# Kernel optimization log

Hardware: AMD Instinct MI355X
Metric: run time of the kernel (lower is better)

The kernel has to match this reference:

```python
import jax, jax.numpy as jnp
import numpy as np

B, IN, H, OUT = 256, 512, 1024, 512
S, Wd, SH = 512, 256, 3          # memory_slots, memory_width, shift_range
P_READ = Wd + 2 + SH + 1         # key, beta, gate, shift(3), gamma
P_WRITE = P_READ + 2 * Wd        # + erase, add


def setup_inputs() -> dict:
    key = jax.random.key(0)
    ks = jax.random.split(key, 8)
    sc = 0.02
    return {
        "x": jax.random.normal(ks[0], (B, IN), jnp.float32),
        "W_ih": jax.random.normal(ks[1], (4 * H, IN + Wd), jnp.float32) * sc,
        "b_ih": jnp.zeros((4 * H,), jnp.float32),
        "W_hh": jax.random.normal(ks[2], (4 * H, H), jnp.float32) * sc,
        "b_hh": jnp.zeros((4 * H,), jnp.float32),
        "W_read": jax.random.normal(ks[3], (P_READ, H), jnp.float32) * sc,
        "b_read": jnp.zeros((P_READ,), jnp.float32),
        "W_write": jax.random.normal(ks[4], (P_WRITE, H), jnp.float32) * sc,
        "b_write": jnp.zeros((P_WRITE,), jnp.float32),
        "W_out": jax.random.normal(ks[5], (OUT, H + Wd), jnp.float32) * sc,
        "b_out": jnp.zeros((OUT,), jnp.float32),
        "mem_bias": jax.random.normal(ks[6], (S, Wd), jnp.float32) * sc,
    }


def _content_address(key_v, beta, memory):
    # cosine similarity of key [B,Wd] vs memory [B,S,Wd], eps=1e-8 like torch
    num = jnp.einsum('bw,bsw->bs', key_v, memory)
    kn = jnp.maximum(jnp.linalg.norm(key_v, axis=1, keepdims=True), 1e-8)
    mn = jnp.maximum(jnp.linalg.norm(memory, axis=2), 1e-8)
    sim = num / (kn * mn) * beta[:, None]
    return jax.nn.softmax(sim, axis=1)


def _address(p, prev_w, memory):
    # content_and_location addressing for a single head
    key_v = p[:, :Wd]
    beta = jax.nn.softplus(p[:, Wd])
    gate = jax.nn.sigmoid(p[:, Wd + 1])
    shift = jax.nn.softmax(p[:, Wd + 2:Wd + 2 + SH], axis=1)
    gamma = 1.0 + jax.nn.softplus(p[:, Wd + 2 + SH])
    cw = _content_address(key_v, beta, memory)
    g = gate[:, None]
    gw = g * cw + (1.0 - g) * prev_w  # interpolation gate
    # circular shift: shifted[pos] = s0*w[pos-1] + s1*w[pos] + s2*w[pos+1]
    sw = (shift[:, 0:1] * jnp.roll(gw, 1, axis=1)
          + shift[:, 1:2] * gw
          + shift[:, 2:3] * jnp.roll(gw, -1, axis=1))
    sp = sw ** gamma[:, None]  # sharpening
    return sp / (jnp.sum(sp, axis=1, keepdims=True) + 1e-6)


def reference(x, W_ih, b_ih, W_hh, b_hh, W_read, b_read, W_write, b_write, W_out, b_out, mem_bias):
    Bb = x.shape[0]
    # init_state (prev_state=None path)
    memory = jnp.broadcast_to(mem_bias[None], (Bb, S, Wd))
    w0 = jnp.zeros((Bb, S), x.dtype).at[:, 0].set(1.0)
    rv = jnp.zeros((Bb, Wd), x.dtype)
    h = jnp.zeros((Bb, H), x.dtype)
    c = jnp.zeros((Bb, H), x.dtype)
    # LSTMCell controller
    inp = jnp.concatenate([x, rv], axis=1)
    gates = inp @ W_ih.T + b_ih + h @ W_hh.T + b_hh
    i, f, g, o = jnp.split(gates, 4, axis=1)
    c = jax.nn.sigmoid(f) * c + jax.nn.sigmoid(i) * jnp.tanh(g)
    h = jax.nn.sigmoid(o) * jnp.tanh(c)
    # read head addressing (1 head)
    rp = h @ W_read.T + b_read
    read_w = _address(rp, w0, memory)
    # write head addressing + erase/add (1 head)
    wp = h @ W_write.T + b_write
    write_w = _address(wp, w0, memory)
    erase = jax.nn.sigmoid(wp[:, P_READ:P_READ + Wd])
    add = jnp.tanh(wp[:, P_READ + Wd:])
    memory = memory * (1.0 - write_w[:, :, None] * erase[:, None, :]) + write_w[:, :, None] * add[:, None, :]
    # read after write
    rv = jnp.einsum('bsw,bs->bw', memory, read_w)
    out = jnp.concatenate([h, rv], axis=1) @ W_out.T + b_out
    return out
```

## Files before the change

### kernel.cpp

```cpp
#include <hip/hip_runtime.h>
#include <hip/hip_bf16.h>
#include <math.h>

#define BB   256
#define INW  512
#define HH   1024
#define OUTW 512
#define SS   512
#define WD   256
#define P_READ  262
#define P_WRITE 774
#define RW_LD   1056
#define W_OFF   272

typedef __attribute__((ext_vector_type(8))) short bf16x8;
typedef __attribute__((ext_vector_type(4))) float f32x4;

__device__ __forceinline__ float sigmoidf(float x) { return 1.f / (1.f + expf(-x)); }
__device__ __forceinline__ float softplusf(float x) { return (x > 20.f) ? x : log1pf(expf(x)); }

#define N_WIH (3072*512)
#define N_WRW (RW_LD*1024)
#define N_WO  (512*1280)
#define N_X   (256*512)
#define N_MB  (512*256)
#define N_MT  (256*512)
#define N_BIA 3072
#define N_BRW RW_LD
#define N_TOT (N_WIH+N_WRW+N_WO+N_X+N_MB+N_MT+N_BIA+N_BRW)
#define NB_ELEM ((N_TOT + 255) / 256)

__global__ __launch_bounds__(256)
void convert_all(const float* __restrict__ W_ih, const float* __restrict__ b_ih,
                 const float* __restrict__ b_hh,
                 const float* __restrict__ W_read, const float* __restrict__ b_read,
                 const float* __restrict__ W_write, const float* __restrict__ b_write,
                 const float* __restrict__ W_out, const float* __restrict__ x,
                 const float* __restrict__ mem,
                 __hip_bfloat16* __restrict__ Wih_c, __hip_bfloat16* __restrict__ Wrw_p,
                 __hip_bfloat16* __restrict__ Wo_b, __hip_bfloat16* __restrict__ x_b,
                 __hip_bfloat16* __restrict__ mem_b, __hip_bfloat16* __restrict__ memT_b,
                 float* __restrict__ bias_c, float* __restrict__ bias_rw,
                 float* __restrict__ mem_norm)
{
    if (blockIdx.x >= NB_ELEM) {
        __shared__ float red[4];
        int s = blockIdx.x - NB_ELEM;
        float v = mem[(size_t)s * WD + threadIdx.x];
        float vv = v * v;
        #pragma unroll
        for (int off = 32; off > 0; off >>= 1) vv += __shfl_down(vv, off, 64);
        int wid = threadIdx.x >> 6;
        if ((threadIdx.x & 63) == 0) red[wid] = vv;
        __syncthreads();
        if (threadIdx.x == 0)
            mem_norm[s] = fmaxf(sqrtf(red[0] + red[1] + red[2] + red[3]), 1e-8f);
        return;
    }
    long i = (long)blockIdx.x * 256 + threadIdx.x;
    if (i >= N_TOT) return;
    if (i < N_WIH) {
        int r = (int)(i >> 9), c = (int)(i & 511);
        int sr = r < 1024 ? r : r + 1024;
        Wih_c[i] = __float2bfloat16(W_ih[(size_t)sr * 768 + c]);
        return;
    }
    i -= N_WIH;
    if (i < N_WRW) {
        int r = (int)(i >> 10), c = (int)(i & 1023);
        float v = 0.f;
        if (r < W_OFF) { if (r < P_READ) v = W_read[(size_t)r * 1024 + c]; }
        else { int wr = r - W_OFF; if (wr < P_WRITE) v = W_write[(size_t)wr * 1024 + c]; }
        Wrw_p[i] = __float2bfloat16(v);
        return;
    }
    i -= N_WRW;
    if (i < N_WO) { Wo_b[i] = __float2bfloat16(W_out[i]); return; }
    i -= N_WO;
    if (i < N_X)  { x_b[i] = __float2bfloat16(x[i]); return; }
    i -= N_X;
    if (i < N_MB) { mem_b[i] = __float2bfloat16(mem[i]); return; }
    i -= N_MB;
    if (i < N_MT) {
        int w = (int)(i >> 9), s = (int)(i & 511);
        memT_b[i] = __float2bfloat16(mem[(size_t)s * 256 + w]);
        return;
    }
    i -= N_MT;
    if (i < N_BIA) {
        int r = (int)i;
        int sr = r < 1024 ? r : r + 1024;
        bias_c[r] = b_ih[sr] + b_hh[sr];
        return;
    }
    i -= N_BIA;
    {
        int r = (int)i;
        float v = 0.f;
        if (r < W_OFF) { if (r < P_READ) v = b_read[r]; }
        else { int wr = r - W_OFF; if (wr < P_WRITE) v = b_write[wr]; }
        bias_rw[r] = v;
    }
}

__global__ __launch_bounds__(64)
void gemm_gates(const __hip_bfloat16* __restrict__ x_b,
                const __hip_bfloat16* __restrict__ Wih_c,
                const float* __restrict__ bias_c,
                __hip_bfloat16* __restrict__ hrv)
{
    const int l = threadIdx.x;
    const int bn = blockIdx.x * 16;
    const int bm = blockIdx.y * 16;
    const int r = l & 15, q = l >> 4;
    const __hip_bfloat16* aptr = x_b + (size_t)(bm + r) * INW + q * 8;
    const __hip_bfloat16* bi = Wih_c + (size_t)(bn + r) * INW + q * 8;
    const __hip_bfloat16* bg = bi + (size_t)1024 * INW;
    const __hip_bfloat16* bo = bi + (size_t)2048 * INW;
    f32x4 ai = {0.f,0.f,0.f,0.f}, ag = ai, ao = ai;
    #pragma unroll
    for (int k = 0; k < INW; k += 32) {
        bf16x8 a = *reinterpret_cast<const bf16x8*>(aptr + k);
        ai = __builtin_amdgcn_mfma_f32_16x16x32_bf16(a, *reinterpret_cast<const bf16x8*>(bi + k), ai, 0, 0, 0);
        ag = __builtin_amdgcn_mfma_f32_16x16x32_bf16(a, *reinterpret_cast<const bf16x8*>(bg + k), ag, 0, 0, 0);
        ao = __builtin_amdgcn_mfma_f32_16x16x32_bf16(a, *reinterpret_cast<const bf16x8*>(bo + k), ao, 0, 0, 0);
    }
    const int j = bn + r;
    const float bii = bias_c[j], big = bias_c[1024 + j], bio = bias_c[2048 + j];
    #pragma unroll
    for (int jj = 0; jj < 4; ++jj) {
        int b = bm + q * 4 + jj;
        float gi = ai[jj] + bii, gg = ag[jj] + big, go = ao[jj] + bio;
        float c = sigmoidf(gi) * tanhf(gg);
        hrv[(size_t)b * 1280 + j] = __float2bfloat16(sigmoidf(go) * tanhf(c));
    }
}

__global__ __launch_bounds__(64)
void gemm_mfma(const __hip_bfloat16* __restrict__ A, int lda,
               const __hip_bfloat16* __restrict__ B, int ldb,
               const float* __restrict__ bias,
               float* __restrict__ C, int ldc, int K,
               __hip_bfloat16* __restrict__ kcopy)
{
    const int l = threadIdx.x;
    const int bn = blockIdx.x * 16;
    const int bm = blockIdx.y * 16;
    const int r = l & 15, q = l >> 4;
    const __hip_bfloat16* aptr = A + (size_t)(bm + r) * lda + q * 8;
    const __hip_bfloat16* bptr = B + (size_t)(bn + r) * ldb + q * 8;
    const int K2 = (K >> 6) << 5;
    f32x4 acc0 = {0.f,0.f,0.f,0.f}, acc1 = acc0;
    #pragma unroll 4
    for (int k = 0; k < K2; k += 32)
        acc0 = __builtin_amdgcn_mfma_f32_16x16x32_bf16(
            *reinterpret_cast<const bf16x8*>(aptr + k),
            *reinterpret_cast<const bf16x8*>(bptr + k), acc0, 0, 0, 0);
    #pragma unroll 4
    for (int k = K2; k < K; k += 32)
        acc1 = __builtin_amdgcn_mfma_f32_16x16x32_bf16(
            *reinterpret_cast<const bf16x8*>(aptr + k),
            *reinterpret_cast<const bf16x8*>(bptr + k), acc1, 0, 0, 0);
    const int col = bn + r;
    const float bv = bias ? bias[col] : 0.f;
    #pragma unroll
    for (int j = 0; j < 4; ++j) {
        int m = bm + q * 4 + j;
        float v = acc0[j] + acc1[j] + bv;
        C[(size_t)m * ldc + col] = v;
        if (kcopy) {
            if (col < WD)
                kcopy[(size_t)m * WD + col] = __float2bfloat16(v);
            else if (col >= W_OFF && col < W_OFF + WD)
                kcopy[(size_t)(256 + m) * WD + (col - W_OFF)] = __float2bfloat16(v);
        }
    }
}

__device__ __forceinline__ void redpair_sum(float& a, float& b, volatile float* redA, volatile float* redB) {
    #pragma unroll
    for (int off = 32; off > 0; off >>= 1) { a += __shfl_down(a, off, 64); b += __shfl_down(b, off, 64); }
    int wid = threadIdx.x >> 6;
    __syncthreads();
    if ((threadIdx.x & 63) == 0) { redA[wid] = a; redB[wid] = b; }
    __syncthreads();
    a = redA[0]+redA[1]+redA[2]+redA[3]+redA[4]+redA[5]+redA[6]+redA[7];
    b = redB[0]+redB[1]+redB[2]+redB[3]+redB[4]+redB[5]+redB[6]+redB[7];
}
__device__ __forceinline__ void redpair_max(float& a, float& b, volatile float* redA, volatile float* redB) {
    #pragma unroll
    for (int off = 32; off > 0; off >>= 1) { a = fmaxf(a, __shfl_down(a, off, 64)); b = fmaxf(b, __shfl_down(b, off, 64)); }
    int wid = threadIdx.x >> 6;
    __syncthreads();
    if ((threadIdx.x & 63) == 0) { redA[wid] = a; redB[wid] = b; }
    __syncthreads();
    a = fmaxf(fmaxf(fmaxf(redA[0],redA[1]),fmaxf(redA[2],redA[3])),fmaxf(fmaxf(redA[4],redA[5]),fmaxf(redA[6],redA[7])));
    b = fmaxf(fmaxf(fmaxf(redB[0],redB[1]),fmaxf(redB[2],redB[3])),fmaxf(fmaxf(redB[4],redB[5]),fmaxf(redB[6],redB[7])));
}

__global__ __launch_bounds__(512)
void address_fused(const float* __restrict__ rpwp, const float* __restrict__ num,
                   const float* __restrict__ mem_norm,
                   __hip_bfloat16* __restrict__ A12, float* __restrict__ t3)
{
    const int b = blockIdx.x;
    const int t = threadIdx.x;
    const float* pr = rpwp + (size_t)b * RW_LD;
    const float* pw = pr + W_OFF;

    __shared__ float redA[8], redB[8];
    __shared__ float bufr[SS], bufw[SS];

    float beta_r  = softplusf(pr[WD]);
    float gate_r  = sigmoidf(pr[WD + 1]);
    float r0 = pr[WD+2], r1 = pr[WD+3], r2 = pr[WD+4];
    float rmx = fmaxf(r0, fmaxf(r1, r2));
    float re0 = expf(r0-rmx), re1 = expf(r1-rmx), re2 = expf(r2-rmx);
    float rinv = 1.f / (re0+re1+re2);
    float shr0 = re0*rinv, shr1 = re1*rinv, shr2 = re2*rinv;
    float gamma_r = 1.f + softplusf(pr[WD + 5]);

    float beta_w  = softplusf(pw[WD]);
    float gate_w  = sigmoidf(pw[WD + 1]);
    float w0 = pw[WD+2], w1 = pw[WD+3], w2 = pw[WD+4];
    float wmx = fmaxf(w0, fmaxf(w1, w2));
    float we0 = expf(w0-wmx), we1 = expf(w1-wmx), we2 = expf(w2-wmx);
    float winv = 1.f / (we0+we1+we2);
    float shw0 = we0*winv, shw1 = we1*winv, shw2 = we2*winv;
    float gamma_w = 1.f + softplusf(pw[WD + 5]);

    {
        float kv = (t < WD) ? pr[t] : pw[t - WD];
        float vv = kv * kv;
        #pragma unroll
        for (int off = 32; off > 0; off >>= 1) vv += __shfl_down(vv, off, 64);
        int wid = t >> 6;
        if ((t & 63) == 0) redA[wid] = vv;
        __syncthreads();
    }
    float knr = fmaxf(sqrtf(redA[0]+redA[1]+redA[2]+redA[3]), 1e-8f);
    float knw = fmaxf(sqrtf(redA[4]+redA[5]+redA[6]+redA[7]), 1e-8f);
    __syncthreads();

    float mni = 1.f / mem_norm[t];
    float sim_r = num[(size_t)b * SS + t]         * mni / knr * beta_r;
    float sim_w = num[(size_t)(256 + b) * SS + t] * mni / knw * beta_w;

    float mr = sim_r, mw = sim_w;
    redpair_max(mr, mw, redA, redB);
    float exr = expf(sim_r - mr), exw = expf(sim_w - mw);
    float sr = exr, sw = exw;
    redpair_sum(sr, sw, redA, redB);
    float cwr = exr / sr, cww = exw / sw;

    float onehot = (t == 0) ? 1.f : 0.f;
    float gwr = gate_r * cwr + (1.f - gate_r) * onehot;
    float gww = gate_w * cww + (1.f - gate_w) * onehot;
    __syncthreads();
    bufr[t] = gwr; bufw[t] = gww;
    __syncthreads();

    int tm = (t + SS - 1) & (SS - 1), tp = (t + 1) & (SS - 1);
    float swr = shr0 * bufr[tm] + shr1 * gwr + shr2 * bufr[tp];
    float sww = shw0 * bufw[tm] + shw1 * gww + shw2 * bufw[tp];

    float spr = powf(swr, gamma_r), spw = powf(sww, gamma_w);
    float ssr = spr, ssw = spw;
    redpair_sum(ssr, ssw, redA, redB);
    float rfin = spr / (ssr + 1e-6f);
    float wfin = spw / (ssw + 1e-6f);

    float prod = rfin * wfin;
    A12[(size_t)b * SS + t] = __float2bfloat16(rfin);
    A12[(size_t)(256 + b) * SS + t] = __float2bfloat16(prod);
    float tp3 = prod, dummy = 0.f;
    redpair_sum(tp3, dummy, redA, redB);
    if (t == 0) t3[b] = tp3;
}

__global__ __launch_bounds__(64)
void gemm_t12rv(const __hip_bfloat16* __restrict__ A12,
                const __hip_bfloat16* __restrict__ memT_b,
                const float* __restrict__ rpwp, const float* __restrict__ t3,
                __hip_bfloat16* __restrict__ hrv)
{
    const int l = threadIdx.x;
    const int bn = blockIdx.x * 16;
    const int bm = blockIdx.y * 16;
    const int r = l & 15, q = l >> 4;
    const __hip_bfloat16* a1 = A12 + (size_t)(bm + r) * SS + q * 8;
    const __hip_bfloat16* a2 = a1 + (size_t)256 * SS;
    const __hip_bfloat16* bp = memT_b + (size_t)(bn + r) * SS + q * 8;
    f32x4 acc1 = {0.f,0.f,0.f,0.f}, acc2 = acc1;
    #pragma unroll
    for (int k = 0; k < SS; k += 32) {
        bf16x8 bb = *reinterpret_cast<const bf16x8*>(bp + k);
        acc1 = __builtin_amdgcn_mfma_f32_16x16x32_bf16(*reinterpret_cast<const bf16x8*>(a1 + k), bb, acc1, 0, 0, 0);
        acc2 = __builtin_amdgcn_mfma_f32_16x16x32_bf16(*reinterpret_cast<const bf16x8*>(a2 + k), bb, acc2, 0, 0, 0);
    }
    const int w = bn + r;
    #pragma unroll
    for (int j = 0; j < 4; ++j) {
        int b = bm + q * 4 + j;
        const float* row = rpwp + (size_t)b * RW_LD;
        float e = sigmoidf(row[W_OFF + P_READ + w]);
        float a = tanhf(row[W_OFF + P_READ + WD + w]);
        float rv = acc1[j] - e * acc2[j] + a * t3[b];
        hrv[(size_t)b * 1280 + 1024 + w] = __float2bfloat16(rv);
    }
}

extern "C" void kernel_launch(void* const* d_in, const int* in_sizes, int n_in,
                              void* d_out, int out_size, void* d_ws, size_t ws_size,
                              hipStream_t stream)
{
    const float* x       = (const float*)d_in[0];
    const float* W_ih    = (const float*)d_in[1];
    const float* b_ih    = (const float*)d_in[2];
    const float* b_hh    = (const float*)d_in[4];
    const float* W_read  = (const float*)d_in[5];
    const float* b_read  = (const float*)d_in[6];
    const float* W_write = (const float*)d_in[7];
    const float* b_write = (const float*)d_in[8];
    const float* W_out   = (const float*)d_in[9];
    const float* b_out   = (const float*)d_in[10];
    const float* mem     = (const float*)d_in[11];

    float* ws = (float*)d_ws;
    float* rpwp     = ws;
    float* num      = ws + 270336;
    float* bias_c   = ws + 532480;
    float* bias_rw  = ws + 535552;
    float* mem_norm = ws + 536608;
    float* t3       = ws + 537120;
    __hip_bfloat16* bfb = (__hip_bfloat16*)(ws + 537376);
    __hip_bfloat16* x_b    = bfb;
    __hip_bfloat16* Wih_c  = bfb + 131072;
    __hip_bfloat16* Wrw_p  = bfb + 1703936;
    __hip_bfloat16* Wo_b   = bfb + 2785280;
    __hip_bfloat16* mem_b  = bfb + 3440640;
    __hip_bfloat16* memT_b = bfb + 3571712;
    __hip_bfloat16* A12    = bfb + 3702784;
    __hip_bfloat16* hrv    = bfb + 3964928;
    __hip_bfloat16* keys   = bfb + 4292608;
    float* out = (float*)d_out;

    convert_all<<<NB_ELEM + SS, 256, 0, stream>>>(
        W_ih, b_ih, b_hh, W_read, b_read, W_write, b_write, W_out, x, mem,
        Wih_c, Wrw_p, Wo_b, x_b, mem_b, memT_b, bias_c, bias_rw, mem_norm);
    gemm_gates<<<dim3(64, 16), 64, 0, stream>>>(x_b, Wih_c, bias_c, hrv);
    gemm_mfma<<<dim3(66, 16), 64, 0, stream>>>(hrv, 1280, Wrw_p, HH, bias_rw,
                                               rpwp, RW_LD, HH, keys);
    gemm_mfma<<<dim3(32, 32), 64, 0, stream>>>(keys, WD, mem_b, WD, nullptr,
                                               num, SS, WD, nullptr);
    address_fused<<<BB, 512, 0, stream>>>(rpwp, num, mem_norm, A12, t3);
    gemm_t12rv<<<dim3(16, 16), 64, 0, stream>>>(A12, memT_b, rpwp, t3, hrv);
    gemm_mfma<<<dim3(32, 16), 64, 0, stream>>>(hrv, 1280, Wo_b, 1280, b_out,
                                               out, OUTW, 1280, nullptr);
}
```

Before: 67.96 us.

## Fuse all stages into one cooperative persistent kernel with grid syncs

Replaces the seven-kernel pipeline with a single cooperative kernel of 256 blocks of 512 threads. Stages are separated by grid.sync: conversion, gate GEMM, read/write projection GEMM, per-batch addressing with in-block content dot products and read-vector computation, then output GEMM accumulation. This removes launch gaps and intermediate buffers such as num, A12 and t3, and computes the similarity and read products with scalar FMAs instead of MFMA tiles. In exchange it pays grid-wide barrier costs and uses only 256 blocks, which may leave many CUs idle during the GEMM stages.

Result: slower. 224.1 us (+229.7%).

```diff
diff --git a/kernel.cpp b/kernel.cpp
--- a/kernel.cpp
+++ b/kernel.cpp
@@ -1,6 +1,9 @@
 #include <hip/hip_runtime.h>
 #include <hip/hip_bf16.h>
+#include <hip/hip_cooperative_groups.h>
 #include <math.h>
+
+namespace cg = cooperative_groups;
 
 #define BB   256
 #define INW  512
@@ -13,11 +16,23 @@
 #define RW_LD   1056
 #define W_OFF   272
 
+#define NBLK 256
+#define NTHR 512
+#define GRIDTH (NBLK * NTHR)
+
 typedef __attribute__((ext_vector_type(8))) short bf16x8;
 typedef __attribute__((ext_vector_type(4))) float f32x4;
 
 __device__ __forceinline__ float sigmoidf(float x) { return 1.f / (1.f + expf(-x)); }
 __device__ __forceinline__ float softplusf(float x) { return (x > 20.f) ? x : log1pf(expf(x)); }
+__device__ __forceinline__ float b2f(short s) {
+    union { float f; unsigned u; } c; c.u = ((unsigned)(unsigned short)s) << 16; return c.f;
+}
+__device__ __forceinline__ float wave_sum(float v) {
+    #pragma unroll
+    for (int off = 32; off > 0; off >>= 1) v += __shfl_down(v, off, 64);
+    return v;
+}
 
 #define N_WIH (3072*512)
 #define N_WRW (RW_LD*1024)
@@ -28,285 +43,323 @@
 #define N_BIA 3072
 #define N_BRW RW_LD
 #define N_TOT (N_WIH+N_WRW+N_WO+N_X+N_MB+N_MT+N_BIA+N_BRW)
-#define NB_ELEM ((N_TOT + 255) / 256)
-
-__global__ __launch_bounds__(256)
-void convert_all(const float* __restrict__ W_ih, const float* __restrict__ b_ih,
-                 const float* __restrict__ b_hh,
-                 const float* __restrict__ W_read, const float* __restrict__ b_read,
-                 const float* __restrict__ W_write, const float* __restrict__ b_write,
-                 const float* __restrict__ W_out, const float* __restrict__ x,
-                 const float* __restrict__ mem,
-                 __hip_bfloat16* __restrict__ Wih_c, __hip_bfloat16* __restrict__ Wrw_p,
-                 __hip_bfloat16* __restrict__ Wo_b, __hip_bfloat16* __restrict__ x_b,
-                 __hip_bfloat16* __restrict__ mem_b, __hip_bfloat16* __restrict__ memT_b,
-                 float* __restrict__ bias_c, float* __restrict__ bias_rw,
-                 float* __restrict__ mem_norm)
+
+struct Params {
+    const float *x, *W_ih, *b_ih, *b_hh, *W_read, *b_read, *W_write, *b_write, *W_out, *b_out, *mem;
+    float *rpwp, *bias_c, *bias_rw, *mem_norm, *out;
+    __hip_bfloat16 *x_b, *Wih_c, *Wrw_p, *Wo_b, *mem_b, *memT_b, *hrv;
+};
+
+__device__ __forceinline__ void st_bf2(__hip_bfloat16* dst, float a, float b) {
+    __hip_bfloat162 h; h.x = __float2bfloat16(a); h.y = __float2bfloat16(b);
+    *reinterpret_cast<__hip_bfloat162*>(dst) = h;
+}
+
+__device__ __forceinline__ void tile_gemm(const __hip_bfloat16* __restrict__ A, int lda,
+                                          const __hip_bfloat16* __restrict__ B, int ldb,
+                                          int kofs, int K, const float* __restrict__ bias,
+                                          float* __restrict__ C, int ldc,
+                                          int bm, int bn, int lane, bool accum)
 {
-    if (blockIdx.x >= NB_ELEM) {
-        __shared__ float red[4];
-        int s = blockIdx.x - NB_ELEM;
-        float v = mem[(size_t)s * WD + threadIdx.x];
-        float vv = v * v;
-        #pragma unroll
-        for (int off = 32; off > 0; off >>= 1) vv += __shfl_down(vv, off, 64);
-        int wid = threadIdx.x >> 6;
-        if ((threadIdx.x & 63) == 0) red[wid] = vv;
-        __syncthreads();
-        if (threadIdx.x == 0)
-            mem_norm[s] = fmaxf(sqrtf(red[0] + red[1] + red[2] + red[3]), 1e-8f);
-        return;
-    }
-    long i = (long)blockIdx.x * 256 + threadIdx.x;
-    if (i >= N_TOT) return;
-    if (i < N_WIH) {
-        int r = (int)(i >> 9), c = (int)(i & 511);
-        int sr = r < 1024 ? r : r + 1024;
-        Wih_c[i] = __float2bfloat16(W_ih[(size_t)sr * 768 + c]);
-        return;
-    }
-    i -= N_WIH;
-    if (i < N_WRW) {
-        int r = (int)(i >> 10), c = (int)(i & 1023);
-        float v = 0.f;
-        if (r < W_OFF) { if (r < P_READ) v = W_read[(size_t)r * 1024 + c]; }
-        else { int wr = r - W_OFF; if (wr < P_WRITE) v = W_write[(size_t)wr * 1024 + c]; }
-        Wrw_p[i] = __float2bfloat16(v);
-        return;
-    }
-    i -= N_WRW;
-    if (i < N_WO) { Wo_b[i] = __float2bfloat16(W_out[i]); return; }
-    i -= N_WO;
-    if (i < N_X)  { x_b[i] = __float2bfloat16(x[i]); return; }
-    i -= N_X;
-    if (i < N_MB) { mem_b[i] = __float2bfloat16(mem[i]); return; }
-    i -= N_MB;
-    if (i < N_MT) {
-        int w = (int)(i >> 9), s = (int)(i & 511);
-        memT_b[i] = __float2bfloat16(mem[(size_t)s * 256 + w]);
-        return;
-    }
-    i -= N_MT;
-    if (i < N_BIA) {
-        int r = (int)i;
-        int sr = r < 1024 ? r : r + 1024;
-        bias_c[r] = b_ih[sr] + b_hh[sr];
-        return;
-    }
-    i -= N_BIA;
-    {
-        int r = (int)i;
-        float v = 0.f;
-        if (r < W_OFF) { if (r < P_READ) v = b_read[r]; }
-        else { int wr = r - W_OFF; if (wr < P_WRITE) v = b_write[wr]; }
-        bias_rw[r] = v;
-    }
-}
-
-__global__ __launch_bounds__(64)
-void gemm_gates(const __hip_bfloat16* __restrict__ x_b,
-                const __hip_bfloat16* __restrict__ Wih_c,
-                const float* __restrict__ bias_c,
-                __hip_bfloat16* __restrict__ hrv)
-{
-    const int l = threadIdx.x;
-    const int bn = blockIdx.x * 16;
-    const int bm = blockIdx.y * 16;
-    const int r = l & 15, q = l >> 4;
-    const __hip_bfloat16* aptr = x_b + (size_t)(bm + r) * INW + q * 8;
-    const __hip_bfloat16* bi = Wih_c + (size_t)(bn + r) * INW + q * 8;
-    const __hip_bfloat16* bg = bi + (size_t)1024 * INW;
-    const __hip_bfloat16* bo = bi + (size_t)2048 * INW;
-    f32x4 ai = {0.f,0.f,0.f,0.f}, ag = ai, ao = ai;
-    #pragma unroll
-    for (int k = 0; k < INW; k += 32) {
-        bf16x8 a = *reinterpret_cast<const bf16x8*>(aptr + k);
-        ai = __builtin_amdgcn_mfma_f32_16x16x32_bf16(a, *reinterpret_cast<const bf16x8*>(bi + k), ai, 0, 0, 0);
-        ag = __builtin_amdgcn_mfma_f32_16x16x32_bf16(a, *reinterpret_cast<const bf16x8*>(bg + k), ag, 0, 0, 0);
-        ao = __builtin_amdgcn_mfma_f32_16x16x32_bf16(a, *reinterpret_cast<const bf16x8*>(bo + k), ao, 0, 0, 0);
-    }
-    const int j = bn + r;
-    const float bii = bias_c[j], big = bias_c[1024 + j], bio = bias_c[2048 + j];
-    #pragma unroll
-    for (int jj = 0; jj < 4; ++jj) {
-        int b = bm + q * 4 + jj;
-        float gi = ai[jj] + bii, gg = ag[jj] + big, go = ao[jj] + bio;
-        float c = sigmoidf(gi) * tanhf(gg);
-        hrv[(size_t)b * 1280 + j] = __float2bfloat16(sigmoidf(go) * tanhf(c));
-    }
-}
-
-__global__ __launch_bounds__(64)
-void gemm_mfma(const __hip_bfloat16* __restrict__ A, int lda,
-               const __hip_bfloat16* __restrict__ B, int ldb,
-               const float* __restrict__ bias,
-               float* __restrict__ C, int ldc, int K,
-               __hip_bfloat16* __restrict__ kcopy)
-{
-    const int l = threadIdx.x;
-    const int bn = blockIdx.x * 16;
-    const int bm = blockIdx.y * 16;
-    const int r = l & 15, q = l >> 4;
-    const __hip_bfloat16* aptr = A + (size_t)(bm + r) * lda + q * 8;
-    const __hip_bfloat16* bptr = B + (size_t)(bn + r) * ldb + q * 8;
+    const int r = lane & 15, q = lane >> 4;
+    const __hip_bfloat16* ap = A + (size_t)(bm + r) * lda + kofs + q * 8;
+    const __hip_bfloat16* bp = B + (size_t)(bn + r) * ldb + kofs + q * 8;
     const int K2 = (K >> 6) << 5;
-    f32x4 acc0 = {0.f,0.f,0.f,0.f}, acc1 = acc0;
+    f32x4 a0 = {0.f,0.f,0.f,0.f}, a1 = a0;
     #pragma unroll 4
     for (int k = 0; k < K2; k += 32)
-        acc0 = __builtin_amdgcn_mfma_f32_16x16x32_bf16(
-            *reinterpret_cast<const bf16x8*>(aptr + k),
-            *reinterpret_cast<const bf16x8*>(bptr + k), acc0, 0, 0, 0);
+        a0 = __builtin_amdgcn_mfma_f32_16x16x32_bf16(
+            *reinterpret_cast<const bf16x8*>(ap + k),
+            *reinterpret_cast<const bf16x8*>(bp + k), a0, 0, 0, 0);
     #pragma unroll 4
     for (int k = K2; k < K; k += 32)
-        acc1 = __builtin_amdgcn_mfma_f32_16x16x32_bf16(
-            *reinterpret_cast<const bf16x8*>(aptr + k),
-            *reinterpret_cast<const bf16x8*>(bptr + k), acc1, 0, 0, 0);
+        a1 = __builtin_amdgcn_mfma_f32_16x16x32_bf16(
+            *reinterpret_cast<const bf16x8*>(ap + k),
+            *reinterpret_cast<const bf16x8*>(bp + k), a1, 0, 0, 0);
     const int col = bn + r;
     const float bv = bias ? bias[col] : 0.f;
     #pragma unroll
     for (int j = 0; j < 4; ++j) {
         int m = bm + q * 4 + j;
-        float v = acc0[j] + acc1[j] + bv;
+        float v = a0[j] + a1[j] + bv;
+        if (accum) v += C[(size_t)m * ldc + col];
         C[(size_t)m * ldc + col] = v;
-        if (kcopy) {
-            if (col < WD)
-                kcopy[(size_t)m * WD + col] = __float2bfloat16(v);
-            else if (col >= W_OFF && col < W_OFF + WD)
-                kcopy[(size_t)(256 + m) * WD + (col - W_OFF)] = __float2bfloat16(v);
-        }
-    }
-}
-
-__device__ __forceinline__ void redpair_sum(float& a, float& b, volatile float* redA, volatile float* redB) {
-    #pragma unroll
-    for (int off = 32; off > 0; off >>= 1) { a += __shfl_down(a, off, 64); b += __shfl_down(b, off, 64); }
-    int wid = threadIdx.x >> 6;
-    __syncthreads();
-    if ((threadIdx.x & 63) == 0) { redA[wid] = a; redB[wid] = b; }
-    __syncthreads();
-    a = redA[0]+redA[1]+redA[2]+redA[3]+redA[4]+redA[5]+redA[6]+redA[7];
-    b = redB[0]+redB[1]+redB[2]+redB[3]+redB[4]+redB[5]+redB[6]+redB[7];
-}
-__device__ __forceinline__ void redpair_max(float& a, float& b, volatile float* redA, volatile float* redB) {
-    #pragma unroll
-    for (int off = 32; off > 0; off >>= 1) { a = fmaxf(a, __shfl_down(a, off, 64)); b = fmaxf(b, __shfl_down(b, off, 64)); }
-    int wid = threadIdx.x >> 6;
-    __syncthreads();
-    if ((threadIdx.x & 63) == 0) { redA[wid] = a; redB[wid] = b; }
-    __syncthreads();
-    a = fmaxf(fmaxf(fmaxf(redA[0],redA[1]),fmaxf(redA[2],redA[3])),fmaxf(fmaxf(redA[4],redA[5]),fmaxf(redA[6],redA[7])));
-    b = fmaxf(fmaxf(fmaxf(redB[0],redB[1]),fmaxf(redB[2],redB[3])),fmaxf(fmaxf(redB[4],redB[5]),fmaxf(redB[6],redB[7])));
-}
-
-__global__ __launch_bounds__(512)
-void address_fused(const float* __restrict__ rpwp, const float* __restrict__ num,
-                   const float* __restrict__ mem_norm,
-                   __hip_bfloat16* __restrict__ A12, float* __restrict__ t3)
+    }
+}
+
+__global__ __launch_bounds__(NTHR, 2)
+void mega(Params p)
 {
-    const int b = blockIdx.x;
+    __shared__ float s_red[8], s_red2[8];
+    __shared__ float s_keyr[256], s_keyw[256];
+    __shared__ float s_bufr[512], s_bufw[512];
+    __shared__ float s_p1[512], s_p2[512];
+
+    cg::grid_group grid = cg::this_grid();
     const int t = threadIdx.x;
-    const float* pr = rpwp + (size_t)b * RW_LD;
-    const float* pw = pr + W_OFF;
-
-    __shared__ float redA[8], redB[8];
-    __shared__ float bufr[SS], bufw[SS];
-
-    float beta_r  = softplusf(pr[WD]);
-    float gate_r  = sigmoidf(pr[WD + 1]);
-    float r0 = pr[WD+2], r1 = pr[WD+3], r2 = pr[WD+4];
-    float rmx = fmaxf(r0, fmaxf(r1, r2));
-    float re0 = expf(r0-rmx), re1 = expf(r1-rmx), re2 = expf(r2-rmx);
-    float rinv = 1.f / (re0+re1+re2);
-    float shr0 = re0*rinv, shr1 = re1*rinv, shr2 = re2*rinv;
-    float gamma_r = 1.f + softplusf(pr[WD + 5]);
-
-    float beta_w  = softplusf(pw[WD]);
-    float gate_w  = sigmoidf(pw[WD + 1]);
-    float w0 = pw[WD+2], w1 = pw[WD+3], w2 = pw[WD+4];
-    float wmx = fmaxf(w0, fmaxf(w1, w2));
-    float we0 = expf(w0-wmx), we1 = expf(w1-wmx), we2 = expf(w2-wmx);
-    float winv = 1.f / (we0+we1+we2);
-    float shw0 = we0*winv, shw1 = we1*winv, shw2 = we2*winv;
-    float gamma_w = 1.f + softplusf(pw[WD + 5]);
+    const int lane = t & 63;
+    const int wid = blockIdx.x * 8 + (t >> 6);
 
     {
-        float kv = (t < WD) ? pr[t] : pw[t - WD];
-        float vv = kv * kv;
+        int s = 2 * blockIdx.x + (t >> 8);
+        float v = p.mem[(size_t)s * WD + (t & 255)];
+        float vv = wave_sum(v * v);
+        if ((t & 63) == 0) s_red[t >> 6] = vv;
+        __syncthreads();
+        if (t == 0)   p.mem_norm[s] = fmaxf(sqrtf(s_red[0]+s_red[1]+s_red[2]+s_red[3]), 1e-8f);
+        if (t == 256) p.mem_norm[s] = fmaxf(sqrtf(s_red[4]+s_red[5]+s_red[6]+s_red[7]), 1e-8f);
+
+        const long NP = N_TOT >> 1;
+        for (long ii = (long)blockIdx.x * NTHR + t; ii < NP; ii += GRIDTH) {
+            long i = ii * 2;
+            if (i < N_WIH) {
+                int r = (int)(i >> 9), c = (int)(i & 511);
+                int sr = r < 1024 ? r : r + 1024;
+                const float* s0 = p.W_ih + (size_t)sr * 768 + c;
+                st_bf2(p.Wih_c + i, s0[0], s0[1]);
+                continue;
+            }
+            i -= N_WIH;
+            if (i < N_WRW) {
+                int r = (int)(i >> 10), c = (int)(i & 1023);
+                float a0 = 0.f, a1 = 0.f;
+                if (r < W_OFF) {
+                    if (r < P_READ) { const float* s0 = p.W_read + (size_t)r * 1024 + c; a0 = s0[0]; a1 = s0[1]; }
+                } else {
+                    int wr = r - W_OFF;
+                    if (wr < P_WRITE) { const float* s0 = p.W_write + (size_t)wr * 1024 + c; a0 = s0[0]; a1 = s0[1]; }
+                }
+                st_bf2(p.Wrw_p + i, a0, a1);
+                continue;
+            }
+            i -= N_WRW;
+            if (i < N_WO) { st_bf2(p.Wo_b + i, p.W_out[i], p.W_out[i + 1]); continue; }
+            i -= N_WO;
+            if (i < N_X)  { st_bf2(p.x_b + i, p.x[i], p.x[i + 1]); continue; }
+            i -= N_X;
+            if (i < N_MB) { st_bf2(p.mem_b + i, p.mem[i], p.mem[i + 1]); continue; }
+            i -= N_MB;
+            if (i < N_MT) {
+                int w = (int)(i >> 9), s0 = (int)(i & 511);
+                st_bf2(p.memT_b + i, p.mem[(size_t)s0 * 256 + w], p.mem[(size_t)(s0 + 1) * 256 + w]);
+                continue;
+            }
+            i -= N_MT;
+            if (i < N_BIA) {
+                #pragma unroll
+                for (int u = 0; u < 2; ++u) {
+                    long r = i + u;
+                    long sr = r < 1024 ? r : r + 1024;
+                    p.bias_c[r] = p.b_ih[sr] + p.b_hh[sr];
+                }
+                continue;
+            }
+            i -= N_BIA;
+            {
+                #pragma unroll
+                for (int u = 0; u < 2; ++u) {
+                    long r = i + u;
+                    float v2 = 0.f;
+                    if (r < W_OFF) { if (r < P_READ) v2 = p.b_read[r]; }
+                    else { long wr = r - W_OFF; if (wr < P_WRITE) v2 = p.b_write[wr]; }
+                    p.bias_rw[r] = v2;
+                }
+            }
+        }
+    }
+    grid.sync();
+
+    if (wid < 1024) {
+        const int bn = (wid & 63) * 16;
+        const int bm = (wid >> 6) * 16;
+        const int r = lane & 15, q = lane >> 4;
+        const __hip_bfloat16* ap = p.x_b + (size_t)(bm + r) * INW + q * 8;
+        const __hip_bfloat16* bi = p.Wih_c + (size_t)(bn + r) * INW + q * 8;
+        const __hip_bfloat16* bg = bi + (size_t)1024 * INW;
+        const __hip_bfloat16* bo = bi + (size_t)2048 * INW;
+        f32x4 ai = {0.f,0.f,0.f,0.f}, ag = ai, ao = ai;
         #pragma unroll
-        for (int off = 32; off > 0; off >>= 1) vv += __shfl_down(vv, off, 64);
-        int wid = t >> 6;
-        if ((t & 63) == 0) redA[wid] = vv;
-        __syncthreads();
-    }
-    float knr = fmaxf(sqrtf(redA[0]+redA[1]+redA[2]+redA[3]), 1e-8f);
-    float knw = fmaxf(sqrtf(redA[4]+redA[5]+redA[6]+redA[7]), 1e-8f);
-    __syncthreads();
-
-    float mni = 1.f / mem_norm[t];
-    float sim_r = num[(size_t)b * SS + t]         * mni / knr * beta_r;
-    float sim_w = num[(size_t)(256 + b) * SS + t] * mni / knw * beta_w;
-
-    float mr = sim_r, mw = sim_w;
-    redpair_max(mr, mw, redA, redB);
-    float exr = expf(sim_r - mr), exw = expf(sim_w - mw);
-    float sr = exr, sw = exw;
-    redpair_sum(sr, sw, redA, redB);
-    float cwr = exr / sr, cww = exw / sw;
-
-    float onehot = (t == 0) ? 1.f : 0.f;
-    float gwr = gate_r * cwr + (1.f - gate_r) * onehot;
-    float gww = gate_w * cww + (1.f - gate_w) * onehot;
-    __syncthreads();
-    bufr[t] = gwr; bufw[t] = gww;
-    __syncthreads();
-
-    int tm = (t + SS - 1) & (SS - 1), tp = (t + 1) & (SS - 1);
-    float swr = shr0 * bufr[tm] + shr1 * gwr + shr2 * bufr[tp];
-    float sww = shw0 * bufw[tm] + shw1 * gww + shw2 * bufw[tp];
-
-    float spr = powf(swr, gamma_r), spw = powf(sww, gamma_w);
-    float ssr = spr, ssw = spw;
-    redpair_sum(ssr, ssw, redA, redB);
-    float rfin = spr / (ssr + 1e-6f);
-    float wfin = spw / (ssw + 1e-6f);
-
-    float prod = rfin * wfin;
-    A12[(size_t)b * SS + t] = __float2bfloat16(rfin);
-    A12[(size_t)(256 + b) * SS + t] = __float2bfloat16(prod);
-    float tp3 = prod, dummy = 0.f;
-    redpair_sum(tp3, dummy, redA, redB);
-    if (t == 0) t3[b] = tp3;
-}
-
-__global__ __launch_bounds__(64)
-void gemm_t12rv(const __hip_bfloat16* __restrict__ A12,
-                const __hip_bfloat16* __restrict__ memT_b,
-                const float* __restrict__ rpwp, const float* __restrict__ t3,
-                __hip_bfloat16* __restrict__ hrv)
-{
-    const int l = threadIdx.x;
-    const int bn = blockIdx.x * 16;
-    const int bm = blockIdx.y * 16;
-    const int r = l & 15, q = l >> 4;
-    const __hip_bfloat16* a1 = A12 + (size_t)(bm + r) * SS + q * 8;
-    const __hip_bfloat16* a2 = a1 + (size_t)256 * SS;
-    const __hip_bfloat16* bp = memT_b + (size_t)(bn + r) * SS + q * 8;
-    f32x4 acc1 = {0.f,0.f,0.f,0.f}, acc2 = acc1;
-    #pragma unroll
-    for (int k = 0; k < SS; k += 32) {
-        bf16x8 bb = *reinterpret_cast<const bf16x8*>(bp + k);
-        acc1 = __builtin_amdgcn_mfma_f32_16x16x32_bf16(*reinterpret_cast<const bf16x8*>(a1 + k), bb, acc1, 0, 0, 0);
-        acc2 = __builtin_amdgcn_mfma_f32_16x16x32_bf16(*reinterpret_cast<const bf16x8*>(a2 + k), bb, acc2, 0, 0, 0);
-    }
-    const int w = bn + r;
-    #pragma unroll
-    for (int j = 0; j < 4; ++j) {
-        int b = bm + q * 4 + j;
-        const float* row = rpwp + (size_t)b * RW_LD;
-        float e = sigmoidf(row[W_OFF + P_READ + w]);
-        float a = tanhf(row[W_OFF + P_READ + WD + w]);
-        float rv = acc1[j] - e * acc2[j] + a * t3[b];
-        hrv[(size_t)b * 1280 + 1024 + w] = __float2bfloat16(rv);
+        for (int k = 0; k < INW; k += 32) {
+            bf16x8 a = *reinterpret_cast<const bf16x8*>(ap + k);
+            ai = __builtin_amdgcn_mfma_f32_16x16x32_bf16(a, *reinterpret_cast<const bf16x8*>(bi + k), ai, 0, 0, 0);
+            ag = __builtin_amdgcn_mfma_f32_16x16x32_bf16(a, *reinterpret_cast<const bf16x8*>(bg + k), ag, 0, 0, 0);
+            ao = __builtin_amdgcn_mfma_f32_16x16x32_bf16(a, *reinterpret_cast<const bf16x8*>(bo + k), ao, 0, 0, 0);
+        }
+        const int j = bn + r;
+        const float bii = p.bias_c[j], big = p.bias_c[1024 + j], bio = p.bias_c[2048 + j];
+        #pragma unroll
+        for (int jj = 0; jj < 4; ++jj) {
+            int b = bm + q * 4 + jj;
+            float c = sigmoidf(ai[jj] + bii) * tanhf(ag[jj] + big);
+            p.hrv[(size_t)b * 1280 + j] = __float2bfloat16(sigmoidf(ao[jj] + bio) * tanhf(c));
+        }
+    }
+    grid.sync();
+
+    if (wid < 1056) {
+        int nt = wid % 66, mt = wid / 66;
+        tile_gemm(p.hrv, 1280, p.Wrw_p, 1024, 0, 1024, p.bias_rw,
+                  p.rpwp, RW_LD, mt * 16, nt * 16, lane, false);
+    } else if (wid < 1568) {
+        int o = wid - 1056;
+        int nt = o & 31, mt = o >> 5;
+        tile_gemm(p.hrv, 1280, p.Wo_b, 1280, 0, 1024, p.b_out,
+                  p.out, OUTW, mt * 16, nt * 16, lane, false);
+    }
+    grid.sync();
+
+    {
+        const int b = blockIdx.x;
+        const float* pr = p.rpwp + (size_t)b * RW_LD;
+        const float* pw = pr + W_OFF;
+
+        float kv;
+        if (t < 256) { kv = pr[t]; s_keyr[t] = kv; }
+        else         { kv = pw[t - 256]; s_keyw[t - 256] = kv; }
+        float vv = wave_sum(kv * kv);
+        if ((t & 63) == 0) s_red[t >> 6] = vv;
+        __syncthreads();
+        float knr = fmaxf(sqrtf(s_red[0]+s_red[1]+s_red[2]+s_red[3]), 1e-8f);
+        float knw = fmaxf(sqrtf(s_red[4]+s_red[5]+s_red[6]+s_red[7]), 1e-8f);
+
+        float beta_r = softplusf(pr[WD]);
+        float gate_r = sigmoidf(pr[WD + 1]);
+        float r0 = pr[WD+2], r1 = pr[WD+3], r2 = pr[WD+4];
+        float rmx = fmaxf(r0, fmaxf(r1, r2));
+        float re0 = expf(r0-rmx), re1 = expf(r1-rmx), re2 = expf(r2-rmx);
+        float rinv = 1.f / (re0+re1+re2);
+        float shr0 = re0*rinv, shr1 = re1*rinv, shr2 = re2*rinv;
+        float gamma_r = 1.f + softplusf(pr[WD + 5]);
+
+        float beta_w = softplusf(pw[WD]);
+        float gate_w = sigmoidf(pw[WD + 1]);
+        float w0 = pw[WD+2], w1 = pw[WD+3], w2 = pw[WD+4];
+        float wmx = fmaxf(w0, fmaxf(w1, w2));
+        float we0 = expf(w0-wmx), we1 = expf(w1-wmx), we2 = expf(w2-wmx);
+        float winv = 1.f / (we0+we1+we2);
+        float shw0 = we0*winv, shw1 = we1*winv, shw2 = we2*winv;
+        float gamma_w = 1.f + softplusf(pw[WD + 5]);
+
+        float nr = 0.f, nw = 0.f;
+        {
+            const bf16x8* mrow = reinterpret_cast<const bf16x8*>(p.mem_b + (size_t)t * WD);
+            const float4* kr4 = reinterpret_cast<const float4*>(s_keyr);
+            const float4* kw4 = reinterpret_cast<const float4*>(s_keyw);
+            #pragma unroll 8
+            for (int kk = 0; kk < 32; ++kk) {
+                bf16x8 m8 = mrow[kk];
+                float4 ka = kr4[2*kk], kb = kr4[2*kk+1];
+                float4 wa = kw4[2*kk], wb = kw4[2*kk+1];
+                float m0=b2f(m8[0]),m1=b2f(m8[1]),m2=b2f(m8[2]),m3=b2f(m8[3]);
+                float m4=b2f(m8[4]),m5=b2f(m8[5]),m6=b2f(m8[6]),m7=b2f(m8[7]);
+                nr += ka.x*m0+ka.y*m1+ka.z*m2+ka.w*m3 + kb.x*m4+kb.y*m5+kb.z*m6+kb.w*m7;
+                nw += wa.x*m0+wa.y*m1+wa.z*m2+wa.w*m3 + wb.x*m4+wb.y*m5+wb.z*m6+wb.w*m7;
+            }
+        }
+        float mni = 1.f / p.mem_norm[t];
+        float sim_r = nr * mni / knr * beta_r;
+        float sim_w = nw * mni / knw * beta_w;
+
+        float mr = sim_r, mw = sim_w;
+        {
+            #pragma unroll
+            for (int off = 32; off > 0; off >>= 1) { mr = fmaxf(mr, __shfl_down(mr, off, 64)); mw = fmaxf(mw, __shfl_down(mw, off, 64)); }
+            int widb = t >> 6;
+            __syncthreads();
+            if ((t & 63) == 0) { s_red[widb] = mr; s_red2[widb] = mw; }
+            __syncthreads();
+            mr = fmaxf(fmaxf(fmaxf(s_red[0],s_red[1]),fmaxf(s_red[2],s_red[3])),fmaxf(fmaxf(s_red[4],s_red[5]),fmaxf(s_red[6],s_red[7])));
+            mw = fmaxf(fmaxf(fmaxf(s_red2[0],s_red2[1]),fmaxf(s_red2[2],s_red2[3])),fmaxf(fmaxf(s_red2[4],s_red2[5]),fmaxf(s_red2[6],s_red2[7])));
+        }
+        float exr = expf(sim_r - mr), exw = expf(sim_w - mw);
+        float sr = exr, sw = exw;
+        {
+            #pragma unroll
+            for (int off = 32; off > 0; off >>= 1) { sr += __shfl_down(sr, off, 64); sw += __shfl_down(sw, off, 64); }
+            int widb = t >> 6;
+            __syncthreads();
+            if ((t & 63) == 0) { s_red[widb] = sr; s_red2[widb] = sw; }
+            __syncthreads();
+            sr = s_red[0]+s_red[1]+s_red[2]+s_red[3]+s_red[4]+s_red[5]+s_red[6]+s_red[7];
+            sw = s_red2[0]+s_red2[1]+s_red2[2]+s_red2[3]+s_red2[4]+s_red2[5]+s_red2[6]+s_red2[7];
+        }
+        float cwr = exr / sr, cww = exw / sw;
+
+        float onehot = (t == 0) ? 1.f : 0.f;
+        float gwr = gate_r * cwr + (1.f - gate_r) * onehot;
+        float gww = gate_w * cww + (1.f - gate_w) * onehot;
+        __syncthreads();
+        s_bufr[t] = gwr; s_bufw[t] = gww;
+        __syncthreads();
+
+        int tm = (t + SS - 1) & (SS - 1), tp = (t + 1) & (SS - 1);
+        float swr = shr0 * s_bufr[tm] + shr1 * gwr + shr2 * s_bufr[tp];
+        float sww = shw0 * s_bufw[tm] + shw1 * gww + shw2 * s_bufw[tp];
+
+        float spr = powf(swr, gamma_r), spw = powf(sww, gamma_w);
+        float ssr = spr, ssw = spw;
+        {
+            #pragma unroll
+            for (int off = 32; off > 0; off >>= 1) { ssr += __shfl_down(ssr, off, 64); ssw += __shfl_down(ssw, off, 64); }
+            int widb = t >> 6;
+            __syncthreads();
+            if ((t & 63) == 0) { s_red[widb] = ssr; s_red2[widb] = ssw; }
+            __syncthreads();
+            ssr = s_red[0]+s_red[1]+s_red[2]+s_red[3]+s_red[4]+s_red[5]+s_red[6]+s_red[7];
+            ssw = s_red2[0]+s_red2[1]+s_red2[2]+s_red2[3]+s_red2[4]+s_red2[5]+s_red2[6]+s_red2[7];
+        }
+        float rfin = spr / (ssr + 1e-6f);
+        float wfin = spw / (ssw + 1e-6f);
+        float prod = rfin * wfin;
+
+        float tp3 = prod, dmy = 0.f;
+        {
+            #pragma unroll
+            for (int off = 32; off > 0; off >>= 1) { tp3 += __shfl_down(tp3, off, 64); dmy += 0.f; }
+            int widb = t >> 6;
+            __syncthreads();
+            if ((t & 63) == 0) s_red[widb] = tp3;
+            __syncthreads();
+            tp3 = s_red[0]+s_red[1]+s_red[2]+s_red[3]+s_red[4]+s_red[5]+s_red[6]+s_red[7];
+        }
+        __syncthreads();
+        s_bufr[t] = rfin; s_bufw[t] = prod;
+        __syncthreads();
+
+        int w = t & 255, half = t >> 8;
+        float p1 = 0.f, p2 = 0.f;
+        {
+            const bf16x8* mTrow = reinterpret_cast<const bf16x8*>(p.memT_b + (size_t)w * SS + half * 256);
+            const float4* br4 = reinterpret_cast<const float4*>(s_bufr + half * 256);
+            const float4* bw4 = reinterpret_cast<const float4*>(s_bufw + half * 256);
+            #pragma unroll 8
+            for (int kk = 0; kk < 32; ++kk) {
+                bf16x8 m8 = mTrow[kk];
+                float4 ra = br4[2*kk], rb = br4[2*kk+1];
+                float4 wa = bw4[2*kk], wb = bw4[2*kk+1];
+                float m0=b2f(m8[0]),m1=b2f(m8[1]),m2=b2f(m8[2]),m3=b2f(m8[3]);
+                float m4=b2f(m8[4]),m5=b2f(m8[5]),m6=b2f(m8[6]),m7=b2f(m8[7]);
+                p1 += ra.x*m0+ra.y*m1+ra.z*m2+ra.w*m3 + rb.x*m4+rb.y*m5+rb.z*m6+rb.w*m7;
+                p2 += wa.x*m0+wa.y*m1+wa.z*m2+wa.w*m3 + wb.x*m4+wb.y*m5+wb.z*m6+wb.w*m7;
+            }
+        }
+        s_p1[t] = p1; s_p2[t] = p2;
+        __syncthreads();
+        if (t < 256) {
+            float P1 = s_p1[t] + s_p1[t + 256];
+            float P2 = s_p2[t] + s_p2[t + 256];
+            float e = sigmoidf(pw[P_READ + t]);
+            float a = tanhf(pw[P_READ + WD + t]);
+            float rv = P1 - e * P2 + a * tp3;
+            p.hrv[(size_t)b * 1280 + 1024 + t] = __float2bfloat16(rv);
+        }
+    }
+    grid.sync();
+
+    if (wid < 512) {
+        int nt = wid & 31, mt = wid >> 5;
+        tile_gemm(p.hrv, 1280, p.Wo_b, 1280, 1024, 256, nullptr,
+                  p.out, OUTW, mt * 16, nt * 16, lane, true);
     }
 }
 
@@ -314,47 +367,34 @@
                               void* d_out, int out_size, void* d_ws, size_t ws_size,
                               hipStream_t stream)
 {
-    const float* x       = (const float*)d_in[0];
-    const float* W_ih    = (const float*)d_in[1];
-    const float* b_ih    = (const float*)d_in[2];
-    const float* b_hh    = (const float*)d_in[4];
-    const float* W_read  = (const float*)d_in[5];
-    const float* b_read  = (const float*)d_in[6];
-    const float* W_write = (const float*)d_in[7];
-    const float* b_write = (const float*)d_in[8];
-    const float* W_out   = (const float*)d_in[9];
-    const float* b_out   = (const float*)d_in[10];
-    const float* mem     = (const float*)d_in[11];
-
     float* ws = (float*)d_ws;
-    float* rpwp     = ws;
-    float* num      = ws + 270336;
-    float* bias_c   = ws + 532480;
-    float* bias_rw  = ws + 535552;
-    float* mem_norm = ws + 536608;
-    float* t3       = ws + 537120;
-    __hip_bfloat16* bfb = (__hip_bfloat16*)(ws + 537376);
-    __hip_bfloat16* x_b    = bfb;
-    __hip_bfloat16* Wih_c  = bfb + 131072;
-    __hip_bfloat16* Wrw_p  = bfb + 1703936;
-    __hip_bfloat16* Wo_b   = bfb + 2785280;
-    __hip_bfloat16* mem_b  = bfb + 3440640;
-    __hip_bfloat16* memT_b = bfb + 3571712;
-    __hip_bfloat16* A12    = bfb + 3702784;
-    __hip_bfloat16* hrv    = bfb + 3964928;
-    __hip_bfloat16* keys   = bfb + 4292608;
-    float* out = (float*)d_out;
-
-    convert_all<<<NB_ELEM + SS, 256, 0, stream>>>(
-        W_ih, b_ih, b_hh, W_read, b_read, W_write, b_write, W_out, x, mem,
-        Wih_c, Wrw_p, Wo_b, x_b, mem_b, memT_b, bias_c, bias_rw, mem_norm);
-    gemm_gates<<<dim3(64, 16), 64, 0, stream>>>(x_b, Wih_c, bias_c, hrv);
-    gemm_mfma<<<dim3(66, 16), 64, 0, stream>>>(hrv, 1280, Wrw_p, HH, bias_rw,
-                                               rpwp, RW_LD, HH, keys);
-    gemm_mfma<<<dim3(32, 32), 64, 0, stream>>>(keys, WD, mem_b, WD, nullptr,
-                                               num, SS, WD, nullptr);
-    address_fused<<<BB, 512, 0, stream>>>(rpwp, num, mem_norm, A12, t3);
-    gemm_t12rv<<<dim3(16, 16), 64, 0, stream>>>(A12, memT_b, rpwp, t3, hrv);
-    gemm_mfma<<<dim3(32, 16), 64, 0, stream>>>(hrv, 1280, Wo_b, 1280, b_out,
-                                               out, OUTW, 1280, nullptr);
-}
+    Params prm;
+    prm.x       = (const float*)d_in[0];
+    prm.W_ih    = (const float*)d_in[1];
+    prm.b_ih    = (const float*)d_in[2];
+    prm.b_hh    = (const float*)d_in[4];
+    prm.W_read  = (const float*)d_in[5];
+    prm.b_read  = (const float*)d_in[6];
+    prm.W_write = (const float*)d_in[7];
+    prm.b_write = (const float*)d_in[8];
+    prm.W_out   = (const float*)d_in[9];
+    prm.b_out   = (const float*)d_in[10];
+    prm.mem     = (const float*)d_in[11];
+
+    prm.rpwp     = ws;
+    prm.bias_c   = ws + 270336;
+    prm.bias_rw  = ws + 273408;
+    prm.mem_norm = ws + 274464;
+    __hip_bfloat16* bfb = (__hip_bfloat16*)(ws + 274976);
+    prm.x_b    = bfb;
+    prm.Wih_c  = bfb + 131072;
+    prm.Wrw_p  = bfb + 1703936;
+    prm.Wo_b   = bfb + 2785280;
+    prm.mem_b  = bfb + 3440640;
+    prm.memT_b = bfb + 3571712;
+    prm.hrv    = bfb + 3702784;
+    prm.out    = (float*)d_out;
+
+    void* kargs[] = { &prm };
+    hipLaunchCooperativeKernel((const void*)mega, dim3(NBLK), dim3(NTHR), kargs, 0, stream);
+}
```
